# Kernel tuning notes

Hardware: AMD Instinct MI355X
Metric: run time of the kernel (lower is better)

Reference implementation:

```python
import jax, jax.numpy as jnp
import numpy as np

N_NODES = 100000
N_EDGES = 1600000
D = 128        # in_dim == hidden_dim (forced by x_j + xe in message)
C = 64         # num_classes
G = 128        # number of graphs in the batch
BN_EPS = 1e-5


def setup_inputs() -> dict:
    key = jax.random.key(0)
    ks = jax.random.split(key, 14)
    s = 0.05
    inp = {
        "x": jax.random.normal(ks[0], (N_NODES, D), dtype=jnp.float32),
        "xe": jax.random.normal(ks[1], (N_EDGES, D), dtype=jnp.float32),
        "edge_index": jax.random.randint(ks[2], (2, N_EDGES), 0, N_NODES, dtype=jnp.int32),
        "batch": jnp.sort(jax.random.randint(ks[3], (N_NODES,), 0, G, dtype=jnp.int32)),
        # layer 0 MySAGEConv params
        "Wl0": jax.random.normal(ks[4], (D, D), dtype=jnp.float32) * s,
        "bl0": jnp.zeros((D,), dtype=jnp.float32),
        "Wr0": jax.random.normal(ks[5], (D, D), dtype=jnp.float32) * s,
        # layer 1 MySAGEConv params
        "Wl1": jax.random.normal(ks[6], (D, D), dtype=jnp.float32) * s,
        "bl1": jnp.zeros((D,), dtype=jnp.float32),
        "Wr1": jax.random.normal(ks[7], (D, D), dtype=jnp.float32) * s,
        # BatchNorm (only applied after non-final layers -> layer 0)
        "gamma0": jnp.ones((D,), dtype=jnp.float32),
        "beta0": jnp.zeros((D,), dtype=jnp.float32),
        # readout projection
        "Wp": jax.random.normal(ks[8], (C, D), dtype=jnp.float32) * s,
        "bp": jnp.zeros((C,), dtype=jnp.float32),
    }
    return inp


def _segment_mean(vals, idx, num_segments):
    s = jax.ops.segment_sum(vals, idx, num_segments=num_segments)
    cnt = jax.ops.segment_sum(jnp.ones((vals.shape[0],), vals.dtype), idx,
                              num_segments=num_segments)
    return s / jnp.clip(cnt, 1.0)[:, None]


def _my_sage_conv(h, xe, src, dst, Wl, bl, Wr):
    # message: relu(x_j + xe); aggregate: scatter-mean at dst; then lin_l + lin_r
    msg = jax.nn.relu(h[src] + xe)                       # [E, D]
    agg = _segment_mean(msg, dst, N_NODES)               # [N, D]
    return agg @ Wl.T + bl + h @ Wr.T


def _batchnorm_train(h, gamma, beta):
    mu = jnp.mean(h, axis=0)
    var = jnp.var(h, axis=0)
    return gamma * (h - mu) * jax.lax.rsqrt(var + BN_EPS) + beta


def reference(x, xe, edge_index, batch,
              Wl0, bl0, Wr0, Wl1, bl1, Wr1,
              gamma0, beta0, Wp, bp):
    src, dst = edge_index[0], edge_index[1]
    # layer 0: conv -> BN -> ReLU
    h = _my_sage_conv(x, xe, src, dst, Wl0, bl0, Wr0)
    h = jax.nn.relu(_batchnorm_train(h, gamma0, beta0))
    # layer 1 (last): conv only
    h = _my_sage_conv(h, xe, src, dst, Wl1, bl1, Wr1)
    # graph readout (global mean pool over pre-proj node features)
    g = _segment_mean(h, batch, G)                       # [G, D]
    # readout projection on nodes
    h = jax.nn.relu(h) @ Wp.T + bp                       # [N, C]
    return h, g
```

## Files before the change

kernel.cpp:

```cpp
#include <hip/hip_runtime.h>

#define N_NODES 100000
#define N_EDGES 1600000
#define DIM 128
#define NCLS 64
#define NG 128
#define BN_EPS 1e-5f

typedef __attribute__((ext_vector_type(8))) short s16x8;
typedef __attribute__((ext_vector_type(4))) float f32x4;
#define MFMA_BF16 __builtin_amdgcn_mfma_f32_16x16x32_bf16

__device__ __forceinline__ void f2hl8(float4 v0, float4 v1, s16x8& h8, s16x8& l8) {
    float vv[8] = {v0.x, v0.y, v0.z, v0.w, v1.x, v1.y, v1.z, v1.w};
#pragma unroll
    for (int i = 0; i < 8; ++i) {
        unsigned u = __float_as_uint(vv[i]);
        short h = (short)(u >> 16);
        float r = vv[i] - __uint_as_float(u & 0xFFFF0000u);
        short l = (short)(__float_as_uint(r) >> 16);
        h8[i] = h;
        l8[i] = l;
    }
}

__global__ void k_hist(const int* __restrict__ dst, int* __restrict__ cnt) {
    int e = blockIdx.x * 256 + threadIdx.x;
    if (e < N_EDGES) atomicAdd(&cnt[dst[e]], 1);
}

__global__ void k_scan1(const int* __restrict__ cnt, int* __restrict__ rowptr,
                        int* __restrict__ bsums) {
    __shared__ int sd[1024];
    int tid = threadIdx.x;
    int i = blockIdx.x * 1024 + tid;
    int v = (i < N_NODES) ? cnt[i] : 0;
    sd[tid] = v;
    __syncthreads();
    for (int off = 1; off < 1024; off <<= 1) {
        int t2 = (tid >= off) ? sd[tid - off] : 0;
        __syncthreads();
        sd[tid] += t2;
        __syncthreads();
    }
    if (i < N_NODES) rowptr[i] = sd[tid] - v;
    if (tid == 1023) bsums[blockIdx.x] = sd[tid];
}

__global__ void k_scan2(int* __restrict__ bsums, int nb) {
    __shared__ int sd[128];
    int t = threadIdx.x;
    int v = (t < nb) ? bsums[t] : 0;
    sd[t] = v;
    __syncthreads();
    for (int off = 1; off < 128; off <<= 1) {
        int u = (t >= off) ? sd[t - off] : 0;
        __syncthreads();
        sd[t] += u;
        __syncthreads();
    }
    if (t < nb) bsums[t] = sd[t] - v;
}

__global__ void k_scan3(int* __restrict__ rowptr, const int* __restrict__ bsums,
                        int* __restrict__ wcur) {
    int i = blockIdx.x * 1024 + threadIdx.x;
    if (i < N_NODES) {
        int v = rowptr[i] + bsums[blockIdx.x];
        rowptr[i] = v;
        wcur[i] = v;
    }
    if (i == N_NODES - 1) rowptr[N_NODES] = N_EDGES;
}

__global__ void k_scatter(const int* __restrict__ src, const int* __restrict__ dst,
                          int* __restrict__ wcur, int2* __restrict__ esort) {
    int e = blockIdx.x * 256 + threadIdx.x;
    if (e < N_EDGES) {
        int d = dst[e];
        int p = atomicAdd(&wcur[d], 1);
        esort[p] = make_int2(e, src[e]);
    }
}

__global__ __launch_bounds__(256) void k_agg(
        const float* __restrict__ F, const float* __restrict__ xe,
        const int* __restrict__ rowptr, const int2* __restrict__ esort,
        float* __restrict__ agg, const float* __restrict__ bnsc, int applyBN) {
    int wid = (blockIdx.x * blockDim.x + threadIdx.x) >> 6;
    int lane = threadIdx.x & 63;
    if (wid >= N_NODES) return;
    int half = lane >> 5;
    int l = lane & 31;
    int p0 = rowptr[wid], p1 = rowptr[wid + 1];
    if (p0 == p1) {
        if (half == 0) {
            float4 z = make_float4(0.f, 0.f, 0.f, 0.f);
            *reinterpret_cast<float4*>(&agg[(size_t)wid * DIM + l * 4]) = z;
        }
        return;
    }
    float4 sc, sh;
    if (applyBN) {
        sc = *reinterpret_cast<const float4*>(&bnsc[l * 4]);
        sh = *reinterpret_cast<const float4*>(&bnsc[DIM + l * 4]);
    }
    float4 acc = make_float4(0.f, 0.f, 0.f, 0.f);
    for (int p = p0; p < p1; p += 4) {
        int q0 = p + half;
        int q1 = p + 2 + half;
        int2 e0 = esort[min(q0, p1 - 1)];
        int2 e1 = esort[min(q1, p1 - 1)];
        float4 a0 = *reinterpret_cast<const float4*>(&F[(size_t)e0.y * DIM + l * 4]);
        float4 b0 = *reinterpret_cast<const float4*>(&xe[(size_t)e0.x * DIM + l * 4]);
        float4 a1 = *reinterpret_cast<const float4*>(&F[(size_t)e1.y * DIM + l * 4]);
        float4 b1 = *reinterpret_cast<const float4*>(&xe[(size_t)e1.x * DIM + l * 4]);
        if (applyBN) {
            a0.x = fmaxf(a0.x * sc.x + sh.x, 0.f); a0.y = fmaxf(a0.y * sc.y + sh.y, 0.f);
            a0.z = fmaxf(a0.z * sc.z + sh.z, 0.f); a0.w = fmaxf(a0.w * sc.w + sh.w, 0.f);
            a1.x = fmaxf(a1.x * sc.x + sh.x, 0.f); a1.y = fmaxf(a1.y * sc.y + sh.y, 0.f);
            a1.z = fmaxf(a1.z * sc.z + sh.z, 0.f); a1.w = fmaxf(a1.w * sc.w + sh.w, 0.f);
        }
        if (q0 < p1) {
            acc.x += fmaxf(a0.x + b0.x, 0.f);
            acc.y += fmaxf(a0.y + b0.y, 0.f);
            acc.z += fmaxf(a0.z + b0.z, 0.f);
            acc.w += fmaxf(a0.w + b0.w, 0.f);
        }
        if (q1 < p1) {
            acc.x += fmaxf(a1.x + b1.x, 0.f);
            acc.y += fmaxf(a1.y + b1.y, 0.f);
            acc.z += fmaxf(a1.z + b1.z, 0.f);
            acc.w += fmaxf(a1.w + b1.w, 0.f);
        }
    }
    acc.x += __shfl_xor(acc.x, 32);
    acc.y += __shfl_xor(acc.y, 32);
    acc.z += __shfl_xor(acc.z, 32);
    acc.w += __shfl_xor(acc.w, 32);
    if (half == 0) {
        float s = 1.f / (float)(p1 - p0);
        acc.x *= s; acc.y *= s; acc.z *= s; acc.w *= s;
        *reinterpret_cast<float4*>(&agg[(size_t)wid * DIM + l * 4]) = acc;
    }
}

__global__ void k_wprep(const float* __restrict__ W, short* __restrict__ hi,
                        short* __restrict__ lo) {
    int tt = threadIdx.x;
    int ct = blockIdx.x;
    int lane = tt & 63, ks = (tt >> 6) & 3;
    int row = ct * 16 + (lane & 15);
    int k0 = ks * 32 + ((lane >> 4) << 3);
    float4 v0 = *reinterpret_cast<const float4*>(&W[(size_t)row * DIM + k0]);
    float4 v1 = *reinterpret_cast<const float4*>(&W[(size_t)row * DIM + k0 + 4]);
    s16x8 h8, l8;
    f2hl8(v0, v1, h8, l8);
    int t = ct * 256 + ks * 64 + lane;
    *reinterpret_cast<s16x8*>(&hi[(size_t)t * 8]) = h8;
    *reinterpret_cast<s16x8*>(&lo[(size_t)t * 8]) = l8;
}

__global__ __launch_bounds__(256) void k_gemm2(
        const float* __restrict__ A, const float* __restrict__ B,
        const short* __restrict__ fW1h, const short* __restrict__ fW1l,
        const short* __restrict__ fW2h, const short* __restrict__ fW2l,
        const float* __restrict__ bias, float* __restrict__ OUT,
        float* __restrict__ bnacc, const float* __restrict__ bnsc,
        int doBN, int bnB) {
    __shared__ char sm[65536];
    const int A_HI = 0, A_LO = 16384, B_HI = 32768, B_LO = 49152;
    int t = threadIdx.x;
    int n0 = blockIdx.x * 64;

    {
        int row = t >> 2;
        int kq = t & 3;
        int n = n0 + row; if (n > N_NODES - 1) n = N_NODES - 1;
        const float* ap = &A[(size_t)n * DIM + kq * 32];
        const float* bp_ = &B[(size_t)n * DIM + kq * 32];
        int sw = (row & 7) << 4;
#pragma unroll
        for (int j = 0; j < 4; ++j) {
            int koffB = kq * 64 + j * 16;
            int addr = row * 256 + (koffB ^ sw);
            float4 v0 = *reinterpret_cast<const float4*>(ap + j * 8);
            float4 v1 = *reinterpret_cast<const float4*>(ap + j * 8 + 4);
            s16x8 h8, l8;
            f2hl8(v0, v1, h8, l8);
            *reinterpret_cast<s16x8*>(sm + A_HI + addr) = h8;
            *reinterpret_cast<s16x8*>(sm + A_LO + addr) = l8;

            float4 u0 = *reinterpret_cast<const float4*>(bp_ + j * 8);
            float4 u1 = *reinterpret_cast<const float4*>(bp_ + j * 8 + 4);
            if (bnB) {
                int k = kq * 32 + j * 8;
                float4 sc0 = *reinterpret_cast<const float4*>(&bnsc[k]);
                float4 sh0 = *reinterpret_cast<const float4*>(&bnsc[DIM + k]);
                float4 sc1 = *reinterpret_cast<const float4*>(&bnsc[k + 4]);
                float4 sh1 = *reinterpret_cast<const float4*>(&bnsc[DIM + k + 4]);
                u0.x = fmaxf(u0.x * sc0.x + sh0.x, 0.f);
                u0.y = fmaxf(u0.y * sc0.y + sh0.y, 0.f);
                u0.z = fmaxf(u0.z * sc0.z + sh0.z, 0.f);
                u0.w = fmaxf(u0.w * sc0.w + sh0.w, 0.f);
                u1.x = fmaxf(u1.x * sc1.x + sh1.x, 0.f);
                u1.y = fmaxf(u1.y * sc1.y + sh1.y, 0.f);
                u1.z = fmaxf(u1.z * sc1.z + sh1.z, 0.f);
                u1.w = fmaxf(u1.w * sc1.w + sh1.w, 0.f);
            }
            s16x8 bh8, bl8;
            f2hl8(u0, u1, bh8, bl8);
            *reinterpret_cast<s16x8*>(sm + B_HI + addr) = bh8;
            *reinterpret_cast<s16x8*>(sm + B_LO + addr) = bl8;
        }
    }
    __syncthreads();

    int w = t >> 6;
    int l = t & 63;
    f32x4 acc[8];
#pragma unroll
    for (int ct = 0; ct < 8; ++ct) acc[ct] = (f32x4){0.f, 0.f, 0.f, 0.f};

    const s16x8* w1h = (const s16x8*)fW1h;
    const s16x8* w1l = (const s16x8*)fW1l;
    const s16x8* w2h = (const s16x8*)fW2h;
    const s16x8* w2l = (const s16x8*)fW2l;
    int arow = w * 16 + (l & 15);
    int asw = (arow & 7) << 4;
#pragma unroll
    for (int ks = 0; ks < 4; ++ks) {
        int koffB = ks * 64 + ((l >> 4) << 4);
        int aaddr = arow * 256 + (koffB ^ asw);
        s16x8 ah = *reinterpret_cast<const s16x8*>(sm + A_HI + aaddr);
        s16x8 al = *reinterpret_cast<const s16x8*>(sm + A_LO + aaddr);
        s16x8 bh = *reinterpret_cast<const s16x8*>(sm + B_HI + aaddr);
        s16x8 bl = *reinterpret_cast<const s16x8*>(sm + B_LO + aaddr);
        int fb = ks * 64 + l;
#pragma unroll
        for (int ct = 0; ct < 8; ++ct) {
            int fi = ct * 256 + fb;
            s16x8 wh1 = w1h[fi], wl1 = w1l[fi];
            s16x8 wh2 = w2h[fi], wl2 = w2l[fi];
            acc[ct] = MFMA_BF16(ah, wh1, acc[ct], 0, 0, 0);
            acc[ct] = MFMA_BF16(ah, wl1, acc[ct], 0, 0, 0);
            acc[ct] = MFMA_BF16(al, wh1, acc[ct], 0, 0, 0);
            acc[ct] = MFMA_BF16(bh, wh2, acc[ct], 0, 0, 0);
            acc[ct] = MFMA_BF16(bh, wl2, acc[ct], 0, 0, 0);
            acc[ct] = MFMA_BF16(bl, wh2, acc[ct], 0, 0, 0);
        }
    }

    float p1s[8], p2s[8];
    int nbase = n0 + w * 16 + ((l >> 4) << 2);
    int col0 = l & 15;
#pragma unroll
    for (int ct = 0; ct < 8; ++ct) {
        float bj = bias[ct * 16 + col0];
        float s1 = 0.f, s2 = 0.f;
#pragma unroll
        for (int r = 0; r < 4; ++r) {
            int n = nbase + r;
            float h = acc[ct][r] + bj;
            if (n < N_NODES) {
                OUT[(size_t)n * DIM + ct * 16 + col0] = h;
                s1 += h; s2 += h * h;
            }
        }
        p1s[ct] = s1; p2s[ct] = s2;
    }
    if (doBN) {
#pragma unroll
        for (int ct = 0; ct < 8; ++ct) {
            p1s[ct] += __shfl_xor(p1s[ct], 16);
            p1s[ct] += __shfl_xor(p1s[ct], 32);
            p2s[ct] += __shfl_xor(p2s[ct], 16);
            p2s[ct] += __shfl_xor(p2s[ct], 32);
        }
        __syncthreads();
        float* red1 = (float*)sm;
        float* red2 = (float*)(sm + 2048);
        if (l < 16) {
#pragma unroll
            for (int ct = 0; ct < 8; ++ct) {
                red1[w * 128 + ct * 16 + l] = p1s[ct];
                red2[w * 128 + ct * 16 + l] = p2s[ct];
            }
        }
        __syncthreads();
        if (t < 128) {
            float s1 = red1[t] + red1[128 + t] + red1[256 + t] + red1[384 + t];
            float s2 = red2[t] + red2[128 + t] + red2[256 + t] + red2[384 + t];
            atomicAdd(&bnacc[t], s1);
            atomicAdd(&bnacc[128 + t], s2);
        }
    }
}

__global__ void k_bnfinal(const float* __restrict__ bnacc, const float* __restrict__ gamma,
                          const float* __restrict__ beta, float* __restrict__ bnsc) {
    int d = threadIdx.x;
    if (d < DIM) {
        float mu = bnacc[d] / (float)N_NODES;
        float var = bnacc[128 + d] / (float)N_NODES - mu * mu;
        float rstd = rsqrtf(var + BN_EPS);
        float sc = gamma[d] * rstd;
        bnsc[d] = sc;
        bnsc[128 + d] = beta[d] - mu * sc;
    }
}

__global__ void k_pool(const float* __restrict__ H1, const int* __restrict__ batch,
                       float* __restrict__ gout) {
    __shared__ float red[4][128];
    int g = blockIdx.x;
    int t = threadIdx.x;
    int d = t & 127;
    int sl = t >> 7;
    int lo = 0, hi = N_NODES;
    while (lo < hi) { int m = (lo + hi) >> 1; if (batch[m] < g) lo = m + 1; else hi = m; }
    int s = lo;
    lo = 0; hi = N_NODES;
    while (lo < hi) { int m = (lo + hi) >> 1; if (batch[m] < g + 1) lo = m + 1; else hi = m; }
    int e = lo;
    float sum = 0.f;
    for (int n = s + sl; n < e; n += 4) sum += H1[(size_t)n * DIM + d];
    red[sl][d] = sum;
    __syncthreads();
    if (t < 128) {
        float tot = red[0][d] + red[1][d] + red[2][d] + red[3][d];
        gout[g * DIM + d] = tot / (float)max(e - s, 1);
    }
}

__global__ __launch_bounds__(256) void k_proj(
        const float* __restrict__ H1, const short* __restrict__ fWph,
        const short* __restrict__ fWpl, const float* __restrict__ bp,
        float* __restrict__ OUT) {
    __shared__ char sm[32768];
    const int A_HI = 0, A_LO = 16384;
    int t = threadIdx.x;
    int n0 = blockIdx.x * 64;
    {
        int row = t >> 2;
        int kq = t & 3;
        int n = n0 + row; if (n > N_NODES - 1) n = N_NODES - 1;
        const float* ap = &H1[(size_t)n * DIM + kq * 32];
        int sw = (row & 7) << 4;
#pragma unroll
        for (int j = 0; j < 4; ++j) {
            int koffB = kq * 64 + j * 16;
            int addr = row * 256 + (koffB ^ sw);
            float4 v0 = *reinterpret_cast<const float4*>(ap + j * 8);
            float4 v1 = *reinterpret_cast<const float4*>(ap + j * 8 + 4);
            v0.x = fmaxf(v0.x, 0.f); v0.y = fmaxf(v0.y, 0.f);
            v0.z = fmaxf(v0.z, 0.f); v0.w = fmaxf(v0.w, 0.f);
            v1.x = fmaxf(v1.x, 0.f); v1.y = fmaxf(v1.y, 0.f);
            v1.z = fmaxf(v1.w, 0.f) == v1.w ? v1.z : v1.z;
            v1.z = fmaxf(v1.z, 0.f); v1.w = fmaxf(v1.w, 0.f);
            s16x8 h8, l8;
            f2hl8(v0, v1, h8, l8);
            *reinterpret_cast<s16x8*>(sm + A_HI + addr) = h8;
            *reinterpret_cast<s16x8*>(sm + A_LO + addr) = l8;
        }
    }
    __syncthreads();

    int w = t >> 6;
    int l = t & 63;
    f32x4 acc[4];
#pragma unroll
    for (int ct = 0; ct < 4; ++ct) acc[ct] = (f32x4){0.f, 0.f, 0.f, 0.f};
    const s16x8* wph = (const s16x8*)fWph;
    const s16x8* wpl = (const s16x8*)fWpl;
    int arow = w * 16 + (l & 15);
    int asw = (arow & 7) << 4;
#pragma unroll
    for (int ks = 0; ks < 4; ++ks) {
        int koffB = ks * 64 + ((l >> 4) << 4);
        int aaddr = arow * 256 + (koffB ^ asw);
        s16x8 ah = *reinterpret_cast<const s16x8*>(sm + A_HI + aaddr);
        s16x8 al = *reinterpret_cast<const s16x8*>(sm + A_LO + aaddr);
        int fb = ks * 64 + l;
#pragma unroll
        for (int ct = 0; ct < 4; ++ct) {
            int fi = ct * 256 + fb;
            s16x8 wh = wph[fi], wl = wpl[fi];
            acc[ct] = MFMA_BF16(ah, wh, acc[ct], 0, 0, 0);
            acc[ct] = MFMA_BF16(ah, wl, acc[ct], 0, 0, 0);
            acc[ct] = MFMA_BF16(al, wh, acc[ct], 0, 0, 0);
        }
    }
    int nbase = n0 + w * 16 + ((l >> 4) << 2);
    int col0 = l & 15;
#pragma unroll
    for (int ct = 0; ct < 4; ++ct) {
        float bj = bp[ct * 16 + col0];
#pragma unroll
        for (int r = 0; r < 4; ++r) {
            int n = nbase + r;
            if (n < N_NODES)
                OUT[(size_t)n * NCLS + ct * 16 + col0] = acc[ct][r] + bj;
        }
    }
}

extern "C" void kernel_launch(void* const* d_in, const int* in_sizes, int n_in,
                              void* d_out, int out_size, void* d_ws, size_t ws_size,
                              hipStream_t stream) {
    (void)in_sizes; (void)n_in; (void)out_size; (void)ws_size;
    const float* x     = (const float*)d_in[0];
    const float* xe    = (const float*)d_in[1];
    const int*   eidx  = (const int*)d_in[2];
    const int*   batch = (const int*)d_in[3];
    const float* Wl0   = (const float*)d_in[4];
    const float* bl0   = (const float*)d_in[5];
    const float* Wr0   = (const float*)d_in[6];
    const float* Wl1   = (const float*)d_in[7];
    const float* bl1   = (const float*)d_in[8];
    const float* Wr1   = (const float*)d_in[9];
    const float* gamma0 = (const float*)d_in[10];
    const float* beta0  = (const float*)d_in[11];
    const float* Wp    = (const float*)d_in[12];
    const float* bp    = (const float*)d_in[13];
    const int* srcp = eidx;
    const int* dstp = eidx + N_EDGES;

    char* ws = (char*)d_ws;
    size_t off = 0;
    auto carve = [&](size_t bytes) {
        void* p = ws + off;
        off = (off + bytes + 255) & ~(size_t)255;
        return p;
    };
    int*   cnt    = (int*)carve((size_t)N_NODES * 4);
    int*   rowptr = (int*)carve((size_t)(N_NODES + 1) * 4);
    int*   wcur   = (int*)carve((size_t)N_NODES * 4);
    int*   bsums  = (int*)carve(128 * 4);
    float* bnacc  = (float*)carve(256 * 4);
    float* bnsc   = (float*)carve(256 * 4);
    int2*  esort  = (int2*)carve((size_t)N_EDGES * 8);
    float* AGG    = (float*)carve((size_t)N_NODES * DIM * 4);
    float* H      = (float*)carve((size_t)N_NODES * DIM * 4);
    float* H1     = (float*)carve((size_t)N_NODES * DIM * 4);
    short* fWl0h = (short*)carve(16384 * 2);
    short* fWl0l = (short*)carve(16384 * 2);
    short* fWr0h = (short*)carve(16384 * 2);
    short* fWr0l = (short*)carve(16384 * 2);
    short* fWl1h = (short*)carve(16384 * 2);
    short* fWl1l = (short*)carve(16384 * 2);
    short* fWr1h = (short*)carve(16384 * 2);
    short* fWr1l = (short*)carve(16384 * 2);
    short* fWph  = (short*)carve(8192 * 2);
    short* fWpl  = (short*)carve(8192 * 2);

    float* out_h = (float*)d_out;
    float* out_g = out_h + (size_t)N_NODES * NCLS;

    hipMemsetAsync(cnt, 0, (size_t)N_NODES * 4, stream);
    hipMemsetAsync(bnacc, 0, 256 * 4, stream);

    k_wprep<<<8, 256, 0, stream>>>(Wl0, fWl0h, fWl0l);
    k_wprep<<<8, 256, 0, stream>>>(Wr0, fWr0h, fWr0l);
    k_wprep<<<8, 256, 0, stream>>>(Wl1, fWl1h, fWl1l);
    k_wprep<<<8, 256, 0, stream>>>(Wr1, fWr1h, fWr1l);
    k_wprep<<<4, 256, 0, stream>>>(Wp, fWph, fWpl);

    int nb = (N_NODES + 1023) / 1024;
    k_hist<<<(N_EDGES + 255) / 256, 256, 0, stream>>>(dstp, cnt);
    k_scan1<<<nb, 1024, 0, stream>>>(cnt, rowptr, bsums);
    k_scan2<<<1, 128, 0, stream>>>(bsums, nb);
    k_scan3<<<nb, 1024, 0, stream>>>(rowptr, bsums, wcur);
    k_scatter<<<(N_EDGES + 255) / 256, 256, 0, stream>>>(srcp, dstp, wcur, esort);

    int gblocks = (N_NODES + 63) / 64;

    k_agg<<<(N_NODES * 64 + 255) / 256, 256, 0, stream>>>(x, xe, rowptr, esort, AGG,
                                                          bnsc, 0);
    k_gemm2<<<gblocks, 256, 0, stream>>>(AGG, x, fWl0h, fWl0l, fWr0h, fWr0l,
                                         bl0, H, bnacc, bnsc, 1, 0);
    k_bnfinal<<<1, 128, 0, stream>>>(bnacc, gamma0, beta0, bnsc);

    k_agg<<<(N_NODES * 64 + 255) / 256, 256, 0, stream>>>(H, xe, rowptr, esort, AGG,
                                                          bnsc, 1);
    k_gemm2<<<gblocks, 256, 0, stream>>>(AGG, H, fWl1h, fWl1l, fWr1h, fWr1l,
                                         bl1, H1, bnacc, bnsc, 0, 1);

    k_pool<<<NG, 512, 0, stream>>>(H1, batch, out_g);
    k_proj<<<gblocks, 256, 0, stream>>>(H1, fWph, fWpl, bp, out_h);
}
```

Measured before the change: 1.019 ms.

## Load GEMM operands directly into MFMA registers, double rows per block, unroll aggregation

The GEMM and projection kernels drop their LDS staging. Each lane now loads its A/B fragments straight from global memory into registers and converts them to bf16 hi/lo pairs there. Each block covers 128 rows, so every weight fragment load is reused across two row tiles, and the launch count drops accordingly. Separately, the edge aggregation loop processes 8 edges per iteration instead of 4 to put more gathers in flight, and the five weight-prep launches are merged into one. The trade-offs are higher register pressure, and the direct global loads read only 32 bytes per lane per row, so the access pattern is less coalesced.

```diff
diff --git a/kernel.cpp b/kernel.cpp
--- a/kernel.cpp
+++ b/kernel.cpp
@@ -22,6 +22,12 @@
         h8[i] = h;
         l8[i] = l;
     }
+}
+
+__device__ __forceinline__ float4 relu4(float4 v) {
+    v.x = fmaxf(v.x, 0.f); v.y = fmaxf(v.y, 0.f);
+    v.z = fmaxf(v.z, 0.f); v.w = fmaxf(v.w, 0.f);
+    return v;
 }
 
 __global__ void k_hist(const int* __restrict__ dst, int* __restrict__ cnt) {
@@ -106,32 +112,48 @@
         sh = *reinterpret_cast<const float4*>(&bnsc[DIM + l * 4]);
     }
     float4 acc = make_float4(0.f, 0.f, 0.f, 0.f);
-    for (int p = p0; p < p1; p += 4) {
+    for (int p = p0; p < p1; p += 8) {
         int q0 = p + half;
         int q1 = p + 2 + half;
+        int q2 = p + 4 + half;
+        int q3 = p + 6 + half;
         int2 e0 = esort[min(q0, p1 - 1)];
         int2 e1 = esort[min(q1, p1 - 1)];
+        int2 e2 = esort[min(q2, p1 - 1)];
+        int2 e3 = esort[min(q3, p1 - 1)];
         float4 a0 = *reinterpret_cast<const float4*>(&F[(size_t)e0.y * DIM + l * 4]);
         float4 b0 = *reinterpret_cast<const float4*>(&xe[(size_t)e0.x * DIM + l * 4]);
         float4 a1 = *reinterpret_cast<const float4*>(&F[(size_t)e1.y * DIM + l * 4]);
         float4 b1 = *reinterpret_cast<const float4*>(&xe[(size_t)e1.x * DIM + l * 4]);
+        float4 a2 = *reinterpret_cast<const float4*>(&F[(size_t)e2.y * DIM + l * 4]);
+        float4 b2 = *reinterpret_cast<const float4*>(&xe[(size_t)e2.x * DIM + l * 4]);
+        float4 a3 = *reinterpret_cast<const float4*>(&F[(size_t)e3.y * DIM + l * 4]);
+        float4 b3 = *reinterpret_cast<const float4*>(&xe[(size_t)e3.x * DIM + l * 4]);
         if (applyBN) {
             a0.x = fmaxf(a0.x * sc.x + sh.x, 0.f); a0.y = fmaxf(a0.y * sc.y + sh.y, 0.f);
             a0.z = fmaxf(a0.z * sc.z + sh.z, 0.f); a0.w = fmaxf(a0.w * sc.w + sh.w, 0.f);
             a1.x = fmaxf(a1.x * sc.x + sh.x, 0.f); a1.y = fmaxf(a1.y * sc.y + sh.y, 0.f);
             a1.z = fmaxf(a1.z * sc.z + sh.z, 0.f); a1.w = fmaxf(a1.w * sc.w + sh.w, 0.f);
+            a2.x = fmaxf(a2.x * sc.x + sh.x, 0.f); a2.y = fmaxf(a2.y * sc.y + sh.y, 0.f);
+            a2.z = fmaxf(a2.z * sc.z + sh.z, 0.f); a2.w = fmaxf(a2.w * sc.w + sh.w, 0.f);
+            a3.x = fmaxf(a3.x * sc.x + sh.x, 0.f); a3.y = fmaxf(a3.y * sc.y + sh.y, 0.f);
+            a3.z = fmaxf(a3.z * sc.z + sh.z, 0.f); a3.w = fmaxf(a3.w * sc.w + sh.w, 0.f);
         }
         if (q0 < p1) {
-            acc.x += fmaxf(a0.x + b0.x, 0.f);
-            acc.y += fmaxf(a0.y + b0.y, 0.f);
-            acc.z += fmaxf(a0.z + b0.z, 0.f);
-            acc.w += fmaxf(a0.w + b0.w, 0.f);
+            acc.x += fmaxf(a0.x + b0.x, 0.f); acc.y += fmaxf(a0.y + b0.y, 0.f);
+            acc.z += fmaxf(a0.z + b0.z, 0.f); acc.w += fmaxf(a0.w + b0.w, 0.f);
         }
         if (q1 < p1) {
-            acc.x += fmaxf(a1.x + b1.x, 0.f);
-            acc.y += fmaxf(a1.y + b1.y, 0.f);
-            acc.z += fmaxf(a1.z + b1.z, 0.f);
-            acc.w += fmaxf(a1.w + b1.w, 0.f);
+            acc.x += fmaxf(a1.x + b1.x, 0.f); acc.y += fmaxf(a1.y + b1.y, 0.f);
+            acc.z += fmaxf(a1.z + b1.z, 0.f); acc.w += fmaxf(a1.w + b1.w, 0.f);
+        }
+        if (q2 < p1) {
+            acc.x += fmaxf(a2.x + b2.x, 0.f); acc.y += fmaxf(a2.y + b2.y, 0.f);
+            acc.z += fmaxf(a2.z + b2.z, 0.f); acc.w += fmaxf(a2.w + b2.w, 0.f);
+        }
+        if (q3 < p1) {
+            acc.x += fmaxf(a3.x + b3.x, 0.f); acc.y += fmaxf(a3.y + b3.y, 0.f);
+            acc.z += fmaxf(a3.z + b3.z, 0.f); acc.w += fmaxf(a3.w + b3.w, 0.f);
         }
     }
     acc.x += __shfl_xor(acc.x, 32);
@@ -145,10 +167,22 @@
     }
 }
 
-__global__ void k_wprep(const float* __restrict__ W, short* __restrict__ hi,
-                        short* __restrict__ lo) {
+__global__ void k_wprep_all(const float* __restrict__ Wl0, const float* __restrict__ Wr0,
+                            const float* __restrict__ Wl1, const float* __restrict__ Wr1,
+                            const float* __restrict__ Wp,
+                            short* __restrict__ fWl0h, short* __restrict__ fWl0l,
+                            short* __restrict__ fWr0h, short* __restrict__ fWr0l,
+                            short* __restrict__ fWl1h, short* __restrict__ fWl1l,
+                            short* __restrict__ fWr1h, short* __restrict__ fWr1l,
+                            short* __restrict__ fWph, short* __restrict__ fWpl) {
+    int b = blockIdx.x;
+    const float* W; short* hi; short* lo; int ct;
+    if (b < 8)       { W = Wl0; hi = fWl0h; lo = fWl0l; ct = b; }
+    else if (b < 16) { W = Wr0; hi = fWr0h; lo = fWr0l; ct = b - 8; }
+    else if (b < 24) { W = Wl1; hi = fWl1h; lo = fWl1l; ct = b - 16; }
+    else if (b < 32) { W = Wr1; hi = fWr1h; lo = fWr1l; ct = b - 24; }
+    else             { W = Wp;  hi = fWph;  lo = fWpl;  ct = b - 32; }
     int tt = threadIdx.x;
-    int ct = blockIdx.x;
     int lane = tt & 63, ks = (tt >> 6) & 3;
     int row = ct * 16 + (lane & 15);
     int k0 = ks * 32 + ((lane >> 4) << 3);
@@ -168,108 +202,112 @@
         const float* __restrict__ bias, float* __restrict__ OUT,
         float* __restrict__ bnacc, const float* __restrict__ bnsc,
         int doBN, int bnB) {
-    __shared__ char sm[65536];
-    const int A_HI = 0, A_LO = 16384, B_HI = 32768, B_LO = 49152;
-    int t = threadIdx.x;
-    int n0 = blockIdx.x * 64;
-
-    {
-        int row = t >> 2;
-        int kq = t & 3;
-        int n = n0 + row; if (n > N_NODES - 1) n = N_NODES - 1;
-        const float* ap = &A[(size_t)n * DIM + kq * 32];
-        const float* bp_ = &B[(size_t)n * DIM + kq * 32];
-        int sw = (row & 7) << 4;
-#pragma unroll
-        for (int j = 0; j < 4; ++j) {
-            int koffB = kq * 64 + j * 16;
-            int addr = row * 256 + (koffB ^ sw);
-            float4 v0 = *reinterpret_cast<const float4*>(ap + j * 8);
-            float4 v1 = *reinterpret_cast<const float4*>(ap + j * 8 + 4);
-            s16x8 h8, l8;
-            f2hl8(v0, v1, h8, l8);
-            *reinterpret_cast<s16x8*>(sm + A_HI + addr) = h8;
-            *reinterpret_cast<s16x8*>(sm + A_LO + addr) = l8;
-
-            float4 u0 = *reinterpret_cast<const float4*>(bp_ + j * 8);
-            float4 u1 = *reinterpret_cast<const float4*>(bp_ + j * 8 + 4);
-            if (bnB) {
-                int k = kq * 32 + j * 8;
-                float4 sc0 = *reinterpret_cast<const float4*>(&bnsc[k]);
-                float4 sh0 = *reinterpret_cast<const float4*>(&bnsc[DIM + k]);
-                float4 sc1 = *reinterpret_cast<const float4*>(&bnsc[k + 4]);
-                float4 sh1 = *reinterpret_cast<const float4*>(&bnsc[DIM + k + 4]);
-                u0.x = fmaxf(u0.x * sc0.x + sh0.x, 0.f);
-                u0.y = fmaxf(u0.y * sc0.y + sh0.y, 0.f);
-                u0.z = fmaxf(u0.z * sc0.z + sh0.z, 0.f);
-                u0.w = fmaxf(u0.w * sc0.w + sh0.w, 0.f);
-                u1.x = fmaxf(u1.x * sc1.x + sh1.x, 0.f);
-                u1.y = fmaxf(u1.y * sc1.y + sh1.y, 0.f);
-                u1.z = fmaxf(u1.z * sc1.z + sh1.z, 0.f);
-                u1.w = fmaxf(u1.w * sc1.w + sh1.w, 0.f);
-            }
-            s16x8 bh8, bl8;
-            f2hl8(u0, u1, bh8, bl8);
-            *reinterpret_cast<s16x8*>(sm + B_HI + addr) = bh8;
-            *reinterpret_cast<s16x8*>(sm + B_LO + addr) = bl8;
-        }
-    }
-    __syncthreads();
-
-    int w = t >> 6;
-    int l = t & 63;
-    f32x4 acc[8];
-#pragma unroll
-    for (int ct = 0; ct < 8; ++ct) acc[ct] = (f32x4){0.f, 0.f, 0.f, 0.f};
-
+    int t = threadIdx.x, w = t >> 6, l = t & 63;
+    int n0 = blockIdx.x * 128;
+    int r = l & 15, kh = l >> 4;
+    int row0 = n0 + w * 16 + r;
+    int row1 = row0 + 64;
+    int n_0 = min(row0, N_NODES - 1);
+    int n_1 = min(row1, N_NODES - 1);
+
+    f32x4 acc0[8], acc1[8];
+#pragma unroll
+    for (int ct = 0; ct < 8; ++ct) {
+        acc0[ct] = (f32x4){0.f, 0.f, 0.f, 0.f};
+        acc1[ct] = (f32x4){0.f, 0.f, 0.f, 0.f};
+    }
     const s16x8* w1h = (const s16x8*)fW1h;
     const s16x8* w1l = (const s16x8*)fW1l;
     const s16x8* w2h = (const s16x8*)fW2h;
     const s16x8* w2l = (const s16x8*)fW2l;
-    int arow = w * 16 + (l & 15);
-    int asw = (arow & 7) << 4;
+
 #pragma unroll
     for (int ks = 0; ks < 4; ++ks) {
-        int koffB = ks * 64 + ((l >> 4) << 4);
-        int aaddr = arow * 256 + (koffB ^ asw);
-        s16x8 ah = *reinterpret_cast<const s16x8*>(sm + A_HI + aaddr);
-        s16x8 al = *reinterpret_cast<const s16x8*>(sm + A_LO + aaddr);
-        s16x8 bh = *reinterpret_cast<const s16x8*>(sm + B_HI + aaddr);
-        s16x8 bl = *reinterpret_cast<const s16x8*>(sm + B_LO + aaddr);
+        int kb = ks * 32 + kh * 8;
+        float4 va0 = *reinterpret_cast<const float4*>(&A[(size_t)n_0 * DIM + kb]);
+        float4 va1 = *reinterpret_cast<const float4*>(&A[(size_t)n_0 * DIM + kb + 4]);
+        float4 vb0 = *reinterpret_cast<const float4*>(&B[(size_t)n_0 * DIM + kb]);
+        float4 vb1 = *reinterpret_cast<const float4*>(&B[(size_t)n_0 * DIM + kb + 4]);
+        float4 wa0 = *reinterpret_cast<const float4*>(&A[(size_t)n_1 * DIM + kb]);
+        float4 wa1 = *reinterpret_cast<const float4*>(&A[(size_t)n_1 * DIM + kb + 4]);
+        float4 wb0 = *reinterpret_cast<const float4*>(&B[(size_t)n_1 * DIM + kb]);
+        float4 wb1 = *reinterpret_cast<const float4*>(&B[(size_t)n_1 * DIM + kb + 4]);
+        if (bnB) {
+            float4 sc0 = *reinterpret_cast<const float4*>(&bnsc[kb]);
+            float4 sh0 = *reinterpret_cast<const float4*>(&bnsc[DIM + kb]);
+            float4 sc1 = *reinterpret_cast<const float4*>(&bnsc[kb + 4]);
+            float4 sh1 = *reinterpret_cast<const float4*>(&bnsc[DIM + kb + 4]);
+            vb0.x = fmaxf(vb0.x * sc0.x + sh0.x, 0.f);
+            vb0.y = fmaxf(vb0.y * sc0.y + sh0.y, 0.f);
+            vb0.z = fmaxf(vb0.z * sc0.z + sh0.z, 0.f);
+            vb0.w = fmaxf(vb0.w * sc0.w + sh0.w, 0.f);
+            vb1.x = fmaxf(vb1.x * sc1.x + sh1.x, 0.f);
+            vb1.y = fmaxf(vb1.y * sc1.y + sh1.y, 0.f);
+            vb1.z = fmaxf(vb1.z * sc1.z + sh1.z, 0.f);
+            vb1.w = fmaxf(vb1.w * sc1.w + sh1.w, 0.f);
+            wb0.x = fmaxf(wb0.x * sc0.x + sh0.x, 0.f);
+            wb0.y = fmaxf(wb0.y * sc0.y + sh0.y, 0.f);
+            wb0.z = fmaxf(wb0.z * sc0.z + sh0.z, 0.f);
+            wb0.w = fmaxf(wb0.w * sc0.w + sh0.w, 0.f);
+            wb1.x = fmaxf(wb1.x * sc1.x + sh1.x, 0.f);
+            wb1.y = fmaxf(wb1.y * sc1.y + sh1.y, 0.f);
+            wb1.z = fmaxf(wb1.z * sc1.z + sh1.z, 0.f);
+            wb1.w = fmaxf(wb1.w * sc1.w + sh1.w, 0.f);
+        }
+        s16x8 a0h, a0l, b0h, b0l, a1h, a1l, b1h, b1l;
+        f2hl8(va0, va1, a0h, a0l);
+        f2hl8(vb0, vb1, b0h, b0l);
+        f2hl8(wa0, wa1, a1h, a1l);
+        f2hl8(wb0, wb1, b1h, b1l);
         int fb = ks * 64 + l;
 #pragma unroll
         for (int ct = 0; ct < 8; ++ct) {
             int fi = ct * 256 + fb;
             s16x8 wh1 = w1h[fi], wl1 = w1l[fi];
             s16x8 wh2 = w2h[fi], wl2 = w2l[fi];
-            acc[ct] = MFMA_BF16(ah, wh1, acc[ct], 0, 0, 0);
-            acc[ct] = MFMA_BF16(ah, wl1, acc[ct], 0, 0, 0);
-            acc[ct] = MFMA_BF16(al, wh1, acc[ct], 0, 0, 0);
-            acc[ct] = MFMA_BF16(bh, wh2, acc[ct], 0, 0, 0);
-            acc[ct] = MFMA_BF16(bh, wl2, acc[ct], 0, 0, 0);
-            acc[ct] = MFMA_BF16(bl, wh2, acc[ct], 0, 0, 0);
+            acc0[ct] = MFMA_BF16(a0h, wh1, acc0[ct], 0, 0, 0);
+            acc0[ct] = MFMA_BF16(a0h, wl1, acc0[ct], 0, 0, 0);
+            acc0[ct] = MFMA_BF16(a0l, wh1, acc0[ct], 0, 0, 0);
+            acc0[ct] = MFMA_BF16(b0h, wh2, acc0[ct], 0, 0, 0);
+            acc0[ct] = MFMA_BF16(b0h, wl2, acc0[ct], 0, 0, 0);
+            acc0[ct] = MFMA_BF16(b0l, wh2, acc0[ct], 0, 0, 0);
+            acc1[ct] = MFMA_BF16(a1h, wh1, acc1[ct], 0, 0, 0);
+            acc1[ct] = MFMA_BF16(a1h, wl1, acc1[ct], 0, 0, 0);
+            acc1[ct] = MFMA_BF16(a1l, wh1, acc1[ct], 0, 0, 0);
+            acc1[ct] = MFMA_BF16(b1h, wh2, acc1[ct], 0, 0, 0);
+            acc1[ct] = MFMA_BF16(b1h, wl2, acc1[ct], 0, 0, 0);
+            acc1[ct] = MFMA_BF16(b1l, wh2, acc1[ct], 0, 0, 0);
         }
     }
 
     float p1s[8], p2s[8];
-    int nbase = n0 + w * 16 + ((l >> 4) << 2);
     int col0 = l & 15;
+    int nb0 = n0 + w * 16 + (kh << 2);
+    int nb1 = nb0 + 64;
 #pragma unroll
     for (int ct = 0; ct < 8; ++ct) {
         float bj = bias[ct * 16 + col0];
         float s1 = 0.f, s2 = 0.f;
 #pragma unroll
-        for (int r = 0; r < 4; ++r) {
-            int n = nbase + r;
-            float h = acc[ct][r] + bj;
+        for (int rr = 0; rr < 4; ++rr) {
+            int n = nb0 + rr;
+            float h = acc0[ct][rr] + bj;
             if (n < N_NODES) {
                 OUT[(size_t)n * DIM + ct * 16 + col0] = h;
                 s1 += h; s2 += h * h;
             }
+            n = nb1 + rr;
+            h = acc1[ct][rr] + bj;
+            if (n < N_NODES) {
+                OUT[(size_t)n * DIM + ct * 16 + col0] = h;
+                s1 += h; s2 += h * h;
+            }
         }
         p1s[ct] = s1; p2s[ct] = s2;
     }
     if (doBN) {
+        __shared__ float red1[512];
+        __shared__ float red2[512];
 #pragma unroll
         for (int ct = 0; ct < 8; ++ct) {
             p1s[ct] += __shfl_xor(p1s[ct], 16);
@@ -277,9 +315,6 @@
             p2s[ct] += __shfl_xor(p2s[ct], 16);
             p2s[ct] += __shfl_xor(p2s[ct], 32);
         }
-        __syncthreads();
-        float* red1 = (float*)sm;
-        float* red2 = (float*)(sm + 2048);
         if (l < 16) {
 #pragma unroll
             for (int ct = 0; ct < 8; ++ct) {
@@ -337,70 +372,58 @@
         const float* __restrict__ H1, const short* __restrict__ fWph,
         const short* __restrict__ fWpl, const float* __restrict__ bp,
         float* __restrict__ OUT) {
-    __shared__ char sm[32768];
-    const int A_HI = 0, A_LO = 16384;
-    int t = threadIdx.x;
-    int n0 = blockIdx.x * 64;
-    {
-        int row = t >> 2;
-        int kq = t & 3;
-        int n = n0 + row; if (n > N_NODES - 1) n = N_NODES - 1;
-        const float* ap = &H1[(size_t)n * DIM + kq * 32];
-        int sw = (row & 7) << 4;
-#pragma unroll
-        for (int j = 0; j < 4; ++j) {
-            int koffB = kq * 64 + j * 16;
-            int addr = row * 256 + (koffB ^ sw);
-            float4 v0 = *reinterpret_cast<const float4*>(ap + j * 8);
-            float4 v1 = *reinterpret_cast<const float4*>(ap + j * 8 + 4);
-            v0.x = fmaxf(v0.x, 0.f); v0.y = fmaxf(v0.y, 0.f);
-            v0.z = fmaxf(v0.z, 0.f); v0.w = fmaxf(v0.w, 0.f);
-            v1.x = fmaxf(v1.x, 0.f); v1.y = fmaxf(v1.y, 0.f);
-            v1.z = fmaxf(v1.w, 0.f) == v1.w ? v1.z : v1.z;
-            v1.z = fmaxf(v1.z, 0.f); v1.w = fmaxf(v1.w, 0.f);
-            s16x8 h8, l8;
-            f2hl8(v0, v1, h8, l8);
-            *reinterpret_cast<s16x8*>(sm + A_HI + addr) = h8;
-            *reinterpret_cast<s16x8*>(sm + A_LO + addr) = l8;
-        }
-    }
-    __syncthreads();
-
-    int w = t >> 6;
-    int l = t & 63;
-    f32x4 acc[4];
-#pragma unroll
-    for (int ct = 0; ct < 4; ++ct) acc[ct] = (f32x4){0.f, 0.f, 0.f, 0.f};
+    int t = threadIdx.x, w = t >> 6, l = t & 63;
+    int n0 = blockIdx.x * 128;
+    int r = l & 15, kh = l >> 4;
+    int row0 = n0 + w * 16 + r;
+    int row1 = row0 + 64;
+    int n_0 = min(row0, N_NODES - 1);
+    int n_1 = min(row1, N_NODES - 1);
+    f32x4 acc0[4], acc1[4];
+#pragma unroll
+    for (int ct = 0; ct < 4; ++ct) {
+        acc0[ct] = (f32x4){0.f, 0.f, 0.f, 0.f};
+        acc1[ct] = (f32x4){0.f, 0.f, 0.f, 0.f};
+    }
     const s16x8* wph = (const s16x8*)fWph;
     const s16x8* wpl = (const s16x8*)fWpl;
-    int arow = w * 16 + (l & 15);
-    int asw = (arow & 7) << 4;
 #pragma unroll
     for (int ks = 0; ks < 4; ++ks) {
-        int koffB = ks * 64 + ((l >> 4) << 4);
-        int aaddr = arow * 256 + (koffB ^ asw);
-        s16x8 ah = *reinterpret_cast<const s16x8*>(sm + A_HI + aaddr);
-        s16x8 al = *reinterpret_cast<const s16x8*>(sm + A_LO + aaddr);
+        int kb = ks * 32 + kh * 8;
+        float4 va0 = relu4(*reinterpret_cast<const float4*>(&H1[(size_t)n_0 * DIM + kb]));
+        float4 va1 = relu4(*reinterpret_cast<const float4*>(&H1[(size_t)n_0 * DIM + kb + 4]));
+        float4 wa0 = relu4(*reinterpret_cast<const float4*>(&H1[(size_t)n_1 * DIM + kb]));
+        float4 wa1 = relu4(*reinterpret_cast<const float4*>(&H1[(size_t)n_1 * DIM + kb + 4]));
+        s16x8 a0h, a0l, a1h, a1l;
+        f2hl8(va0, va1, a0h, a0l);
+        f2hl8(wa0, wa1, a1h, a1l);
         int fb = ks * 64 + l;
 #pragma unroll
         for (int ct = 0; ct < 4; ++ct) {
             int fi = ct * 256 + fb;
             s16x8 wh = wph[fi], wl = wpl[fi];
-            acc[ct] = MFMA_BF16(ah, wh, acc[ct], 0, 0, 0);
-            acc[ct] = MFMA_BF16(ah, wl, acc[ct], 0, 0, 0);
-            acc[ct] = MFMA_BF16(al, wh, acc[ct], 0, 0, 0);
-        }
-    }
-    int nbase = n0 + w * 16 + ((l >> 4) << 2);
+            acc0[ct] = MFMA_BF16(a0h, wh, acc0[ct], 0, 0, 0);
+            acc0[ct] = MFMA_BF16(a0h, wl, acc0[ct], 0, 0, 0);
+            acc0[ct] = MFMA_BF16(a0l, wh, acc0[ct], 0, 0, 0);
+            acc1[ct] = MFMA_BF16(a1h, wh, acc1[ct], 0, 0, 0);
+            acc1[ct] = MFMA_BF16(a1h, wl, acc1[ct], 0, 0, 0);
+            acc1[ct] = MFMA_BF16(a1l, wh, acc1[ct], 0, 0, 0);
+        }
+    }
     int col0 = l & 15;
+    int nb0 = n0 + w * 16 + (kh << 2);
+    int nb1 = nb0 + 64;
 #pragma unroll
     for (int ct = 0; ct < 4; ++ct) {
         float bj = bp[ct * 16 + col0];
 #pragma unroll
-        for (int r = 0; r < 4; ++r) {
-            int n = nbase + r;
+        for (int rr = 0; rr < 4; ++rr) {
+            int n = nb0 + rr;
             if (n < N_NODES)
-                OUT[(size_t)n * NCLS + ct * 16 + col0] = acc[ct][r] + bj;
+                OUT[(size_t)n * NCLS + ct * 16 + col0] = acc0[ct][rr] + bj;
+            n = nb1 + rr;
+            if (n < N_NODES)
+                OUT[(size_t)n * NCLS + ct * 16 + col0] = acc1[ct][rr] + bj;
         }
     }
 }
@@ -460,11 +483,10 @@
     hipMemsetAsync(cnt, 0, (size_t)N_NODES * 4, stream);
     hipMemsetAsync(bnacc, 0, 256 * 4, stream);
 
-    k_wprep<<<8, 256, 0, stream>>>(Wl0, fWl0h, fWl0l);
-    k_wprep<<<8, 256, 0, stream>>>(Wr0, fWr0h, fWr0l);
-    k_wprep<<<8, 256, 0, stream>>>(Wl1, fWl1h, fWl1l);
-    k_wprep<<<8, 256, 0, stream>>>(Wr1, fWr1h, fWr1l);
-    k_wprep<<<4, 256, 0, stream>>>(Wp, fWph, fWpl);
+    k_wprep_all<<<36, 256, 0, stream>>>(Wl0, Wr0, Wl1, Wr1, Wp,
+                                        fWl0h, fWl0l, fWr0h, fWr0l,
+                                        fWl1h, fWl1l, fWr1h, fWr1l,
+                                        fWph, fWpl);
 
     int nb = (N_NODES + 1023) / 1024;
     k_hist<<<(N_EDGES + 255) / 256, 256, 0, stream>>>(dstp, cnt);
@@ -473,7 +495,7 @@
     k_scan3<<<nb, 1024, 0, stream>>>(rowptr, bsums, wcur);
     k_scatter<<<(N_EDGES + 255) / 256, 256, 0, stream>>>(srcp, dstp, wcur, esort);
 
-    int gblocks = (N_NODES + 63) / 64;
+    int gblocks = (N_NODES + 127) / 128;
 
     k_agg<<<(N_NODES * 64 + 255) / 256, 256, 0, stream>>>(x, xe, rowptr, esort, AGG,
                                                           bnsc, 0);
```

Result: faster. 889.6 us (-12.7%).
